# Optimization experiments

Measured on AMD Instinct MI355X. Metric: run time of the kernel, lower is better.

Reference implementation:

```python
import jax, jax.numpy as jnp
import numpy as np


def setup_inputs() -> dict:
    key = jax.random.key(0)
    k1, k2, k3 = jax.random.split(key, 3)
    B, N, L, H, E = 4, 4, 1024, 8, 64
    queries = jax.random.normal(k1, (B, N, L, H, E), dtype=jnp.float32)
    keys = jax.random.normal(k2, (B, N, L, H, E), dtype=jnp.float32)
    values = jax.random.normal(k3, (B, N, L, H, E), dtype=jnp.float32)
    return {"queries": queries, "keys": keys, "values": values}


def reference(queries, keys, values):
    B, N, L, H, E = queries.shape
    S = values.shape[2]
    scale = 1.0 / jnp.sqrt(jnp.asarray(E, queries.dtype))
    # scores: [B, N, H, L, S]
    scores = jnp.einsum('bnlhe,bnshe->bnhls', queries, keys)
    # causal mask: True above the diagonal (future positions), broadcast over b,n,h
    causal = jnp.triu(jnp.ones((L, S), dtype=bool), k=1)
    scores = jnp.where(causal, -jnp.inf, scores)
    A = jax.nn.softmax(scale * scores, axis=-1)  # dropout p=0.0 -> identity
    V = jnp.einsum('bnhls,bnshd->bnlhd', A, values)
    return V
```

## Files before the change

kernel.cpp:

```cpp
#include <hip/hip_runtime.h>
#include <hip/hip_bf16.h>


typedef __bf16 bf16x8 __attribute__((ext_vector_type(8)));
typedef __bf16 bf16x4 __attribute__((ext_vector_type(4)));
typedef float  f32x4  __attribute__((ext_vector_type(4)));
typedef unsigned u32x2 __attribute__((ext_vector_type(2)));
typedef unsigned u32x4 __attribute__((ext_vector_type(4)));

#define SEQ 1024
#define ROWSTRIDE 512

__device__ inline bf16x8 pack8(float4 a, float4 b) {
    bf16x8 f;
    f[0]=(__bf16)a.x; f[1]=(__bf16)a.y; f[2]=(__bf16)a.z; f[3]=(__bf16)a.w;
    f[4]=(__bf16)b.x; f[5]=(__bf16)b.y; f[6]=(__bf16)b.z; f[7]=(__bf16)b.w;
    return f;
}

__device__ inline bf16x8 pack8s(float4 a, float4 b, float s) {
    bf16x8 f;
    f[0]=(__bf16)(a.x*s); f[1]=(__bf16)(a.y*s); f[2]=(__bf16)(a.z*s); f[3]=(__bf16)(a.w*s);
    f[4]=(__bf16)(b.x*s); f[5]=(__bf16)(b.y*s); f[6]=(__bf16)(b.z*s); f[7]=(__bf16)(b.w*s);
    return f;
}

__device__ inline void lds_barrier() {
    asm volatile("s_waitcnt lgkmcnt(0)\n\ts_barrier" ::: "memory");
}

__device__ inline void swap32(unsigned &a, unsigned &b) {
    asm("v_permlane32_swap_b32 %0, %1" : "+v"(a), "+v"(b));
}
__device__ inline void swap16(unsigned &a, unsigned &b) {
    asm("v_permlane16_swap_b32 %0, %1" : "+v"(a), "+v"(b));
}

__global__ __launch_bounds__(256) void attn_fwd(
    const float* __restrict__ Qg,
    const float* __restrict__ Kg,
    const float* __restrict__ Vg,
    float* __restrict__ Og)
{
    __shared__ __bf16 Kds[2][64][64];
    __shared__ __bf16 Vds[2][64][64];

    const int blk  = blockIdx.x;
    const int pr   = blk >> 7;
    const int head = blk & 127;
    const int h    = head & 7;
    const int bn   = head >> 3;
    const int qts[2] = { pr, 15 - pr };

    const int tid  = threadIdx.x;
    const int wave = tid >> 6;
    const int lane = tid & 63;
    const int quad = lane >> 4;
    const int l15  = lane & 15;
    const int swz  = l15 & 7;

    const size_t base = (size_t)bn * SEQ * ROWSTRIDE + (size_t)h * 64;

    const float kscale = 0.125f * 1.44269504088896f;

    bf16x8 qa[2][2];
    int qrow[2];
    #pragma unroll
    for (int st = 0; st < 2; ++st) {
        qrow[st] = qts[st] * 64 + wave * 16;
        const float* qp = Qg + base + (size_t)(qrow[st] + l15) * ROWSTRIDE + quad * 8;
        #pragma unroll
        for (int t = 0; t < 2; ++t)
            qa[st][t] = pack8s(*(const float4*)(qp + t * 32),
                               *(const float4*)(qp + t * 32 + 4), kscale);
    }

    f32x4 o[2][4];
    float lsum[2];
    #pragma unroll
    for (int st = 0; st < 2; ++st) {
        #pragma unroll
        for (int e = 0; e < 4; ++e) o[st][e] = (f32x4){0.f, 0.f, 0.f, 0.f};
        lsum[st] = 0.f;
    }

    const int sr = tid >> 2, cbk = (tid & 3) << 1;
    const int ve = tid & 63, cbv = (tid >> 6) << 1;

    const int ntiles = qts[1] + 1;

    const float* kbase = Kg + base;
    const float* vbase = Vg + base;

    float4 kpre[4];
    float  vpre[16];
    {
        const float* kp = kbase + (size_t)sr * ROWSTRIDE + (cbk << 3);
        #pragma unroll
        for (int i = 0; i < 4; ++i) kpre[i] = *(const float4*)(kp + i * 4);
        const float* vp = vbase + (size_t)(cbv << 3) * ROWSTRIDE + ve;
        #pragma unroll
        for (int j = 0; j < 16; ++j) vpre[j] = vp[(size_t)j * ROWSTRIDE];
    }

    for (int tile = 0; tile < ntiles; ++tile) {
        const int bb = tile & 1;

        {
            const int rk = sr & 7;
            *(bf16x8*)&Kds[bb][sr][(cbk ^ rk) << 3]       = pack8(kpre[0], kpre[1]);
            *(bf16x8*)&Kds[bb][sr][((cbk + 1) ^ rk) << 3] = pack8(kpre[2], kpre[3]);
            bf16x8 f0, f1;
            #pragma unroll
            for (int jj = 0; jj < 8; ++jj) { f0[jj] = (__bf16)vpre[jj]; f1[jj] = (__bf16)vpre[8 + jj]; }
            const int rv = ve & 7;
            *(bf16x8*)&Vds[bb][ve][(cbv ^ rv) << 3]       = f0;
            *(bf16x8*)&Vds[bb][ve][((cbv + 1) ^ rv) << 3] = f1;
        }

        if (tile + 1 < ntiles) {
            const int s0n = (tile + 1) << 6;
            const float* kp = kbase + (size_t)(s0n + sr) * ROWSTRIDE + (cbk << 3);
            #pragma unroll
            for (int i = 0; i < 4; ++i) kpre[i] = *(const float4*)(kp + i * 4);
            const float* vp = vbase + (size_t)(s0n + (cbv << 3)) * ROWSTRIDE + ve;
            #pragma unroll
            for (int j = 0; j < 16; ++j) vpre[j] = vp[(size_t)j * ROWSTRIDE];
        }

        lds_barrier();

        bf16x8 pf[2][2];
        #pragma unroll
        for (int st = 0; st < 2; ++st) {
            if (tile > qts[st]) continue;
            f32x4 sacc[4];
            __builtin_amdgcn_s_setprio(1);
            #pragma unroll
            for (int c = 0; c < 4; ++c) {
                sacc[c] = (f32x4){0.f, 0.f, 0.f, 0.f};
                #pragma unroll
                for (int t = 0; t < 2; ++t) {
                    bf16x8 kb = *(const bf16x8*)&Kds[bb][c * 16 + l15][((t * 4 + quad) ^ swz) << 3];
                    sacc[c] = __builtin_amdgcn_mfma_f32_16x16x32_bf16(kb, qa[st][t], sacc[c], 0, 0, 0);
                }
            }
            __builtin_amdgcn_s_setprio(0);
            const bool diag = (tile == qts[st]);
            const int qin = wave * 16 + l15;
            float ls = 0.f;
            unsigned U[4][2];
            #pragma unroll
            for (int c = 0; c < 4; ++c) {
                bf16x4 pk;
                #pragma unroll
                for (int r = 0; r < 4; ++r) {
                    float p = __builtin_amdgcn_exp2f(sacc[c][r]);
                    if (diag && (c * 16 + quad * 4 + r > qin)) p = 0.f;
                    ls += p;
                    pk[r] = (__bf16)p;
                }
                u32x2 uu = __builtin_bit_cast(u32x2, pk);
                U[c][0] = uu[0]; U[c][1] = uu[1];
            }
            lsum[st] += ls;
            #pragma unroll
            for (int t = 0; t < 2; ++t) {
                unsigned a0 = U[2 * t][0], a1 = U[2 * t][1];
                unsigned b0 = U[2 * t + 1][0], b1 = U[2 * t + 1][1];
                swap32(a0, b0); swap32(a1, b1);
                swap16(a0, b0); swap16(a1, b1);
                u32x4 w; w[0] = a0; w[1] = a1; w[2] = b0; w[3] = b1;
                pf[st][t] = __builtin_bit_cast(bf16x8, w);
            }
        }

        const bool both = (tile <= qts[0]);
        __builtin_amdgcn_s_setprio(1);
        #pragma unroll
        for (int e = 0; e < 4; ++e) {
            #pragma unroll
            for (int t = 0; t < 2; ++t) {
                bf16x8 vb = *(const bf16x8*)&Vds[bb][e * 16 + l15][((t * 4 + quad) ^ swz) << 3];
                if (both)
                    o[0][e] = __builtin_amdgcn_mfma_f32_16x16x32_bf16(vb, pf[0][t], o[0][e], 0, 0, 0);
                o[1][e] = __builtin_amdgcn_mfma_f32_16x16x32_bf16(vb, pf[1][t], o[1][e], 0, 0, 0);
            }
        }
        __builtin_amdgcn_s_setprio(0);
    }

    #pragma unroll
    for (int st = 0; st < 2; ++st) {
        float s = lsum[st];
        s += __shfl_xor(s, 16);
        s += __shfl_xor(s, 32);
        const float inv_l = 1.f / s;
        float* op = Og + base + (size_t)(qrow[st] + l15) * ROWSTRIDE + quad * 4;
        #pragma unroll
        for (int e = 0; e < 4; ++e) {
            float4 v;
            v.x = o[st][e][0] * inv_l;
            v.y = o[st][e][1] * inv_l;
            v.z = o[st][e][2] * inv_l;
            v.w = o[st][e][3] * inv_l;
            *(float4*)(op + e * 16) = v;
        }
    }
}

extern "C" void kernel_launch(void* const* d_in, const int* in_sizes, int n_in,
                              void* d_out, int out_size, void* d_ws, size_t ws_size,
                              hipStream_t stream) {
    const float* Qg = (const float*)d_in[0];
    const float* Kg = (const float*)d_in[1];
    const float* Vg = (const float*)d_in[2];
    float* Og = (float*)d_out;
    attn_fwd<<<dim3(1024), dim3(256), 0, stream>>>(Qg, Kg, Vg, Og);
}
```

Before: 162.6 us.

## Split paired query tiles into separate blocks with 32-row KV tiles

Replaces the paired-query-tile scheme, where each block handled tiles pr and 15-pr, with one 64-row query tile per block and 2048 blocks. The KV tile shrinks to 32 rows and the V LDS layout and swizzle change to match. Per-wave causal skipping now leaves out fully masked 32-key subtiles. Launch bounds request 8 blocks per CU for higher occupancy. In exchange it loses load balancing between blocks and re-reads K/V once per query tile instead of once per pair.

After: 207.4 us. 1.28x slower.

```diff
diff --git a/kernel.cpp b/kernel.cpp
--- a/kernel.cpp
+++ b/kernel.cpp
@@ -10,6 +10,7 @@
 
 #define SEQ 1024
 #define ROWSTRIDE 512
+#define KVB 32
 
 __device__ inline bf16x8 pack8(float4 a, float4 b) {
     bf16x8 f;
@@ -36,21 +37,20 @@
     asm("v_permlane16_swap_b32 %0, %1" : "+v"(a), "+v"(b));
 }
 
-__global__ __launch_bounds__(256) void attn_fwd(
+__global__ __launch_bounds__(256, 8) void attn_fwd(
     const float* __restrict__ Qg,
     const float* __restrict__ Kg,
     const float* __restrict__ Vg,
     float* __restrict__ Og)
 {
-    __shared__ __bf16 Kds[2][64][64];
-    __shared__ __bf16 Vds[2][64][64];
+    __shared__ __bf16 Kds[2][KVB][64];
+    __shared__ __bf16 Vds[2][64][KVB];
 
     const int blk  = blockIdx.x;
-    const int pr   = blk >> 7;
+    const int qt   = blk >> 7;
     const int head = blk & 127;
     const int h    = head & 7;
     const int bn   = head >> 3;
-    const int qts[2] = { pr, 15 - pr };
 
     const int tid  = threadIdx.x;
     const int wave = tid >> 6;
@@ -58,152 +58,134 @@
     const int quad = lane >> 4;
     const int l15  = lane & 15;
     const int swz  = l15 & 7;
+    const int vswz = (l15 >> 1) & 3;
 
     const size_t base = (size_t)bn * SEQ * ROWSTRIDE + (size_t)h * 64;
 
     const float kscale = 0.125f * 1.44269504088896f;
 
-    bf16x8 qa[2][2];
-    int qrow[2];
-    #pragma unroll
-    for (int st = 0; st < 2; ++st) {
-        qrow[st] = qts[st] * 64 + wave * 16;
-        const float* qp = Qg + base + (size_t)(qrow[st] + l15) * ROWSTRIDE + quad * 8;
+    const int qrow = qt * 64 + wave * 16;
+    bf16x8 qa[2];
+    {
+        const float* qp = Qg + base + (size_t)(qrow + l15) * ROWSTRIDE + quad * 8;
         #pragma unroll
         for (int t = 0; t < 2; ++t)
-            qa[st][t] = pack8s(*(const float4*)(qp + t * 32),
-                               *(const float4*)(qp + t * 32 + 4), kscale);
+            qa[t] = pack8s(*(const float4*)(qp + t * 32),
+                           *(const float4*)(qp + t * 32 + 4), kscale);
     }
 
-    f32x4 o[2][4];
-    float lsum[2];
+    f32x4 o[4];
+    float lsum = 0.f;
     #pragma unroll
-    for (int st = 0; st < 2; ++st) {
-        #pragma unroll
-        for (int e = 0; e < 4; ++e) o[st][e] = (f32x4){0.f, 0.f, 0.f, 0.f};
-        lsum[st] = 0.f;
-    }
-
-    const int sr = tid >> 2, cbk = (tid & 3) << 1;
-    const int ve = tid & 63, cbv = (tid >> 6) << 1;
-
-    const int ntiles = qts[1] + 1;
-
-    const float* kbase = Kg + base;
-    const float* vbase = Vg + base;
-
-    float4 kpre[4];
-    float  vpre[16];
-    {
-        const float* kp = kbase + (size_t)sr * ROWSTRIDE + (cbk << 3);
-        #pragma unroll
-        for (int i = 0; i < 4; ++i) kpre[i] = *(const float4*)(kp + i * 4);
-        const float* vp = vbase + (size_t)(cbv << 3) * ROWSTRIDE + ve;
-        #pragma unroll
-        for (int j = 0; j < 16; ++j) vpre[j] = vp[(size_t)j * ROWSTRIDE];
-    }
+    for (int e = 0; e < 4; ++e) o[e] = (f32x4){0.f, 0.f, 0.f, 0.f};
+
+    const int sr = tid >> 3, kc = tid & 7;
+    const int ve = tid & 63;
+
+    const int ntiles = 2 * qt + 2;
+
+    const float* kp = Kg + base + (size_t)sr * ROWSTRIDE + kc * 8;
+    const float* vp = Vg + base + (size_t)(wave * 8) * ROWSTRIDE + ve;
+
+    float4 kpre[2];
+    float  vpre[8];
+    kpre[0] = *(const float4*)kp;
+    kpre[1] = *(const float4*)(kp + 4);
+    #pragma unroll
+    for (int j = 0; j < 8; ++j) vpre[j] = vp[(size_t)j * ROWSTRIDE];
+    kp += (size_t)KVB * ROWSTRIDE;
+    vp += (size_t)KVB * ROWSTRIDE;
 
     for (int tile = 0; tile < ntiles; ++tile) {
         const int bb = tile & 1;
 
+        *(bf16x8*)&Kds[bb][sr][(kc ^ (sr & 7)) << 3] = pack8(kpre[0], kpre[1]);
         {
-            const int rk = sr & 7;
-            *(bf16x8*)&Kds[bb][sr][(cbk ^ rk) << 3]       = pack8(kpre[0], kpre[1]);
-            *(bf16x8*)&Kds[bb][sr][((cbk + 1) ^ rk) << 3] = pack8(kpre[2], kpre[3]);
-            bf16x8 f0, f1;
-            #pragma unroll
-            for (int jj = 0; jj < 8; ++jj) { f0[jj] = (__bf16)vpre[jj]; f1[jj] = (__bf16)vpre[8 + jj]; }
-            const int rv = ve & 7;
-            *(bf16x8*)&Vds[bb][ve][(cbv ^ rv) << 3]       = f0;
-            *(bf16x8*)&Vds[bb][ve][((cbv + 1) ^ rv) << 3] = f1;
-        }
-
-        if (tile + 1 < ntiles) {
-            const int s0n = (tile + 1) << 6;
-            const float* kp = kbase + (size_t)(s0n + sr) * ROWSTRIDE + (cbk << 3);
-            #pragma unroll
-            for (int i = 0; i < 4; ++i) kpre[i] = *(const float4*)(kp + i * 4);
-            const float* vp = vbase + (size_t)(s0n + (cbv << 3)) * ROWSTRIDE + ve;
-            #pragma unroll
-            for (int j = 0; j < 16; ++j) vpre[j] = vp[(size_t)j * ROWSTRIDE];
+            bf16x8 f0;
+            #pragma unroll
+            for (int jj = 0; jj < 8; ++jj) f0[jj] = (__bf16)vpre[jj];
+            *(bf16x8*)&Vds[bb][ve][(wave ^ ((ve >> 1) & 3)) << 3] = f0;
         }
 
         lds_barrier();
 
-        bf16x8 pf[2][2];
-        #pragma unroll
-        for (int st = 0; st < 2; ++st) {
-            if (tile > qts[st]) continue;
-            f32x4 sacc[4];
+        const int reltile = tile * 32 - qt * 64 - wave * 16;
+        const bool active = reltile < 16;
+
+        bf16x8 pf;
+        if (active) {
+            f32x4 sacc[2];
             __builtin_amdgcn_s_setprio(1);
             #pragma unroll
-            for (int c = 0; c < 4; ++c) {
+            for (int c = 0; c < 2; ++c) {
                 sacc[c] = (f32x4){0.f, 0.f, 0.f, 0.f};
                 #pragma unroll
                 for (int t = 0; t < 2; ++t) {
                     bf16x8 kb = *(const bf16x8*)&Kds[bb][c * 16 + l15][((t * 4 + quad) ^ swz) << 3];
-                    sacc[c] = __builtin_amdgcn_mfma_f32_16x16x32_bf16(kb, qa[st][t], sacc[c], 0, 0, 0);
+                    sacc[c] = __builtin_amdgcn_mfma_f32_16x16x32_bf16(kb, qa[t], sacc[c], 0, 0, 0);
                 }
             }
             __builtin_amdgcn_s_setprio(0);
-            const bool diag = (tile == qts[st]);
-            const int qin = wave * 16 + l15;
+
+            const bool diag = (reltile >= -16);
             float ls = 0.f;
-            unsigned U[4][2];
-            #pragma unroll
-            for (int c = 0; c < 4; ++c) {
+            unsigned U[2][2];
+            #pragma unroll
+            for (int c = 0; c < 2; ++c) {
                 bf16x4 pk;
                 #pragma unroll
                 for (int r = 0; r < 4; ++r) {
                     float p = __builtin_amdgcn_exp2f(sacc[c][r]);
-                    if (diag && (c * 16 + quad * 4 + r > qin)) p = 0.f;
+                    if (diag && (reltile + c * 16 + quad * 4 + r > l15)) p = 0.f;
                     ls += p;
                     pk[r] = (__bf16)p;
                 }
                 u32x2 uu = __builtin_bit_cast(u32x2, pk);
                 U[c][0] = uu[0]; U[c][1] = uu[1];
             }
-            lsum[st] += ls;
-            #pragma unroll
-            for (int t = 0; t < 2; ++t) {
-                unsigned a0 = U[2 * t][0], a1 = U[2 * t][1];
-                unsigned b0 = U[2 * t + 1][0], b1 = U[2 * t + 1][1];
-                swap32(a0, b0); swap32(a1, b1);
-                swap16(a0, b0); swap16(a1, b1);
-                u32x4 w; w[0] = a0; w[1] = a1; w[2] = b0; w[3] = b1;
-                pf[st][t] = __builtin_bit_cast(bf16x8, w);
+            lsum += ls;
+
+            unsigned a0 = U[0][0], a1 = U[0][1];
+            unsigned b0 = U[1][0], b1 = U[1][1];
+            swap32(a0, b0); swap32(a1, b1);
+            swap16(a0, b0); swap16(a1, b1);
+            u32x4 w; w[0] = a0; w[1] = a1; w[2] = b0; w[3] = b1;
+            pf = __builtin_bit_cast(bf16x8, w);
+        }
+
+        if (tile + 1 < ntiles) {
+            kpre[0] = *(const float4*)kp;
+            kpre[1] = *(const float4*)(kp + 4);
+            #pragma unroll
+            for (int j = 0; j < 8; ++j) vpre[j] = vp[(size_t)j * ROWSTRIDE];
+            kp += (size_t)KVB * ROWSTRIDE;
+            vp += (size_t)KVB * ROWSTRIDE;
+        }
+
+        if (active) {
+            __builtin_amdgcn_s_setprio(1);
+            #pragma unroll
+            for (int e = 0; e < 4; ++e) {
+                bf16x8 vb = *(const bf16x8*)&Vds[bb][e * 16 + l15][(quad ^ vswz) << 3];
+                o[e] = __builtin_amdgcn_mfma_f32_16x16x32_bf16(vb, pf, o[e], 0, 0, 0);
             }
-        }
-
-        const bool both = (tile <= qts[0]);
-        __builtin_amdgcn_s_setprio(1);
-        #pragma unroll
-        for (int e = 0; e < 4; ++e) {
-            #pragma unroll
-            for (int t = 0; t < 2; ++t) {
-                bf16x8 vb = *(const bf16x8*)&Vds[bb][e * 16 + l15][((t * 4 + quad) ^ swz) << 3];
-                if (both)
-                    o[0][e] = __builtin_amdgcn_mfma_f32_16x16x32_bf16(vb, pf[0][t], o[0][e], 0, 0, 0);
-                o[1][e] = __builtin_amdgcn_mfma_f32_16x16x32_bf16(vb, pf[1][t], o[1][e], 0, 0, 0);
-            }
-        }
-        __builtin_amdgcn_s_setprio(0);
+            __builtin_amdgcn_s_setprio(0);
+        }
     }
 
-    #pragma unroll
-    for (int st = 0; st < 2; ++st) {
-        float s = lsum[st];
+    {
+        float s = lsum;
         s += __shfl_xor(s, 16);
         s += __shfl_xor(s, 32);
         const float inv_l = 1.f / s;
-        float* op = Og + base + (size_t)(qrow[st] + l15) * ROWSTRIDE + quad * 4;
+        float* op = Og + base + (size_t)(qrow + l15) * ROWSTRIDE + quad * 4;
         #pragma unroll
         for (int e = 0; e < 4; ++e) {
             float4 v;
-            v.x = o[st][e][0] * inv_l;
-            v.y = o[st][e][1] * inv_l;
-            v.z = o[st][e][2] * inv_l;
-            v.w = o[st][e][3] * inv_l;
+            v.x = o[e][0] * inv_l;
+            v.y = o[e][1] * inv_l;
+            v.z = o[e][2] * inv_l;
+            v.w = o[e][3] * inv_l;
             *(float4*)(op + e * 16) = v;
         }
     }
@@ -216,5 +198,5 @@
     const float* Kg = (const float*)d_in[1];
     const float* Vg = (const float*)d_in[2];
     float* Og = (float*)d_out;
-    attn_fwd<<<dim3(1024), dim3(256), 0, stream>>>(Qg, Kg, Vg, Og);
-}
+    attn_fwd<<<dim3(2048), dim3(256), 0, stream>>>(Qg, Kg, Vg, Og);
+}
```

## Replace paired-tile balancing with 128-row query tiles and per-wave causal skipping

Applied to the files above, without the earlier changes.

Each block now handles one contiguous 128-row query tile (32 rows per wave) instead of a balanced pair of 64-row tiles, and loops over 2*qt+2 key tiles. Each wave processes key tiles in 32-column phases and skips phases and PV MFMAs that lie entirely above its diagonal, so K fragments are reused across two query sub-tiles. This drops the front/back pairing that balanced work across blocks. Blocks now carry very different amounts of work, which may leave a long tail of late-running blocks.

Measured after the change: 155.5 us. 4.4% less time.

```diff
diff --git a/kernel.cpp b/kernel.cpp
--- a/kernel.cpp
+++ b/kernel.cpp
@@ -46,11 +46,10 @@
     __shared__ __bf16 Vds[2][64][64];
 
     const int blk  = blockIdx.x;
-    const int pr   = blk >> 7;
+    const int qt   = blk >> 7;
     const int head = blk & 127;
     const int h    = head & 7;
     const int bn   = head >> 3;
-    const int qts[2] = { pr, 15 - pr };
 
     const int tid  = threadIdx.x;
     const int wave = tid >> 6;
@@ -63,45 +62,40 @@
 
     const float kscale = 0.125f * 1.44269504088896f;
 
+    const int qrow = qt * 128 + wave * 32;
     bf16x8 qa[2][2];
-    int qrow[2];
-    #pragma unroll
-    for (int st = 0; st < 2; ++st) {
-        qrow[st] = qts[st] * 64 + wave * 16;
-        const float* qp = Qg + base + (size_t)(qrow[st] + l15) * ROWSTRIDE + quad * 8;
+    #pragma unroll
+    for (int qh = 0; qh < 2; ++qh) {
+        const float* qp = Qg + base + (size_t)(qrow + qh * 16 + l15) * ROWSTRIDE + quad * 8;
         #pragma unroll
         for (int t = 0; t < 2; ++t)
-            qa[st][t] = pack8s(*(const float4*)(qp + t * 32),
+            qa[qh][t] = pack8s(*(const float4*)(qp + t * 32),
                                *(const float4*)(qp + t * 32 + 4), kscale);
     }
 
     f32x4 o[2][4];
-    float lsum[2];
-    #pragma unroll
-    for (int st = 0; st < 2; ++st) {
+    float lsum[2] = {0.f, 0.f};
+    #pragma unroll
+    for (int qh = 0; qh < 2; ++qh)
         #pragma unroll
-        for (int e = 0; e < 4; ++e) o[st][e] = (f32x4){0.f, 0.f, 0.f, 0.f};
-        lsum[st] = 0.f;
-    }
+        for (int e = 0; e < 4; ++e) o[qh][e] = (f32x4){0.f, 0.f, 0.f, 0.f};
 
     const int sr = tid >> 2, cbk = (tid & 3) << 1;
     const int ve = tid & 63, cbv = (tid >> 6) << 1;
 
-    const int ntiles = qts[1] + 1;
-
-    const float* kbase = Kg + base;
-    const float* vbase = Vg + base;
+    const int ntiles = 2 * qt + 2;
+
+    const float* kp = Kg + base + (size_t)sr * ROWSTRIDE + (cbk << 3);
+    const float* vp = Vg + base + (size_t)(cbv << 3) * ROWSTRIDE + ve;
 
     float4 kpre[4];
     float  vpre[16];
-    {
-        const float* kp = kbase + (size_t)sr * ROWSTRIDE + (cbk << 3);
-        #pragma unroll
-        for (int i = 0; i < 4; ++i) kpre[i] = *(const float4*)(kp + i * 4);
-        const float* vp = vbase + (size_t)(cbv << 3) * ROWSTRIDE + ve;
-        #pragma unroll
-        for (int j = 0; j < 16; ++j) vpre[j] = vp[(size_t)j * ROWSTRIDE];
-    }
+    #pragma unroll
+    for (int i = 0; i < 4; ++i) kpre[i] = *(const float4*)(kp + i * 4);
+    #pragma unroll
+    for (int j = 0; j < 16; ++j) vpre[j] = vp[(size_t)j * ROWSTRIDE];
+    kp += (size_t)64 * ROWSTRIDE;
+    vp += (size_t)64 * ROWSTRIDE;
 
     for (int tile = 0; tile < ntiles; ++tile) {
         const int bb = tile & 1;
@@ -119,91 +113,114 @@
         }
 
         if (tile + 1 < ntiles) {
-            const int s0n = (tile + 1) << 6;
-            const float* kp = kbase + (size_t)(s0n + sr) * ROWSTRIDE + (cbk << 3);
             #pragma unroll
             for (int i = 0; i < 4; ++i) kpre[i] = *(const float4*)(kp + i * 4);
-            const float* vp = vbase + (size_t)(s0n + (cbv << 3)) * ROWSTRIDE + ve;
             #pragma unroll
             for (int j = 0; j < 16; ++j) vpre[j] = vp[(size_t)j * ROWSTRIDE];
+            kp += (size_t)64 * ROWSTRIDE;
+            vp += (size_t)64 * ROWSTRIDE;
         }
 
         lds_barrier();
 
+        const int relq = tile * 64 - qrow;
+        const bool active   = relq < 32;
+        const bool hiActive = relq < 0;
+
         bf16x8 pf[2][2];
-        #pragma unroll
-        for (int st = 0; st < 2; ++st) {
-            if (tile > qts[st]) continue;
-            f32x4 sacc[4];
+
+        auto phase = [&](int ph) {
+            f32x4 sacc[2][2];
+            #pragma unroll
+            for (int qh = 0; qh < 2; ++qh)
+                #pragma unroll
+                for (int cl = 0; cl < 2; ++cl) sacc[qh][cl] = (f32x4){0.f, 0.f, 0.f, 0.f};
             __builtin_amdgcn_s_setprio(1);
             #pragma unroll
-            for (int c = 0; c < 4; ++c) {
-                sacc[c] = (f32x4){0.f, 0.f, 0.f, 0.f};
+            for (int cl = 0; cl < 2; ++cl) {
                 #pragma unroll
                 for (int t = 0; t < 2; ++t) {
-                    bf16x8 kb = *(const bf16x8*)&Kds[bb][c * 16 + l15][((t * 4 + quad) ^ swz) << 3];
-                    sacc[c] = __builtin_amdgcn_mfma_f32_16x16x32_bf16(kb, qa[st][t], sacc[c], 0, 0, 0);
+                    bf16x8 kb = *(const bf16x8*)&Kds[bb][(ph * 2 + cl) * 16 + l15][((t * 4 + quad) ^ swz) << 3];
+                    sacc[0][cl] = __builtin_amdgcn_mfma_f32_16x16x32_bf16(kb, qa[0][t], sacc[0][cl], 0, 0, 0);
+                    sacc[1][cl] = __builtin_amdgcn_mfma_f32_16x16x32_bf16(kb, qa[1][t], sacc[1][cl], 0, 0, 0);
                 }
             }
             __builtin_amdgcn_s_setprio(0);
-            const bool diag = (tile == qts[st]);
-            const int qin = wave * 16 + l15;
-            float ls = 0.f;
-            unsigned U[4][2];
-            #pragma unroll
-            for (int c = 0; c < 4; ++c) {
-                bf16x4 pk;
-                #pragma unroll
-                for (int r = 0; r < 4; ++r) {
-                    float p = __builtin_amdgcn_exp2f(sacc[c][r]);
-                    if (diag && (c * 16 + quad * 4 + r > qin)) p = 0.f;
-                    ls += p;
-                    pk[r] = (__bf16)p;
+            const int pm = relq + ph * 32;
+            #pragma unroll
+            for (int qh = 0; qh < 2; ++qh) {
+                unsigned U[2][2];
+                float ls = 0.f;
+                if (pm == 0) {
+                    #pragma unroll
+                    for (int cl = 0; cl < 2; ++cl) {
+                        bf16x4 pk;
+                        #pragma unroll
+                        for (int r = 0; r < 4; ++r) {
+                            float p = __builtin_amdgcn_exp2f(sacc[qh][cl][r]);
+                            if (cl * 16 + quad * 4 + r > qh * 16 + l15) p = 0.f;
+                            ls += p; pk[r] = (__bf16)p;
+                        }
+                        u32x2 uu = __builtin_bit_cast(u32x2, pk);
+                        U[cl][0] = uu[0]; U[cl][1] = uu[1];
+                    }
+                } else {
+                    #pragma unroll
+                    for (int cl = 0; cl < 2; ++cl) {
+                        bf16x4 pk;
+                        #pragma unroll
+                        for (int r = 0; r < 4; ++r) {
+                            float p = __builtin_amdgcn_exp2f(sacc[qh][cl][r]);
+                            ls += p; pk[r] = (__bf16)p;
+                        }
+                        u32x2 uu = __builtin_bit_cast(u32x2, pk);
+                        U[cl][0] = uu[0]; U[cl][1] = uu[1];
+                    }
                 }
-                u32x2 uu = __builtin_bit_cast(u32x2, pk);
-                U[c][0] = uu[0]; U[c][1] = uu[1];
-            }
-            lsum[st] += ls;
-            #pragma unroll
-            for (int t = 0; t < 2; ++t) {
-                unsigned a0 = U[2 * t][0], a1 = U[2 * t][1];
-                unsigned b0 = U[2 * t + 1][0], b1 = U[2 * t + 1][1];
+                lsum[qh] += ls;
+                unsigned a0 = U[0][0], a1 = U[0][1];
+                unsigned b0 = U[1][0], b1 = U[1][1];
                 swap32(a0, b0); swap32(a1, b1);
                 swap16(a0, b0); swap16(a1, b1);
                 u32x4 w; w[0] = a0; w[1] = a1; w[2] = b0; w[3] = b1;
-                pf[st][t] = __builtin_bit_cast(bf16x8, w);
+                pf[qh][ph] = __builtin_bit_cast(bf16x8, w);
             }
-        }
-
-        const bool both = (tile <= qts[0]);
-        __builtin_amdgcn_s_setprio(1);
-        #pragma unroll
-        for (int e = 0; e < 4; ++e) {
-            #pragma unroll
-            for (int t = 0; t < 2; ++t) {
-                bf16x8 vb = *(const bf16x8*)&Vds[bb][e * 16 + l15][((t * 4 + quad) ^ swz) << 3];
-                if (both)
-                    o[0][e] = __builtin_amdgcn_mfma_f32_16x16x32_bf16(vb, pf[0][t], o[0][e], 0, 0, 0);
-                o[1][e] = __builtin_amdgcn_mfma_f32_16x16x32_bf16(vb, pf[1][t], o[1][e], 0, 0, 0);
+        };
+
+        if (active) {
+            phase(0);
+            if (hiActive) phase(1);
+
+            __builtin_amdgcn_s_setprio(1);
+            #pragma unroll
+            for (int e = 0; e < 4; ++e) {
+                bf16x8 vb0 = *(const bf16x8*)&Vds[bb][e * 16 + l15][(quad ^ swz) << 3];
+                o[0][e] = __builtin_amdgcn_mfma_f32_16x16x32_bf16(vb0, pf[0][0], o[0][e], 0, 0, 0);
+                o[1][e] = __builtin_amdgcn_mfma_f32_16x16x32_bf16(vb0, pf[1][0], o[1][e], 0, 0, 0);
+                if (hiActive) {
+                    bf16x8 vb1 = *(const bf16x8*)&Vds[bb][e * 16 + l15][((4 + quad) ^ swz) << 3];
+                    o[0][e] = __builtin_amdgcn_mfma_f32_16x16x32_bf16(vb1, pf[0][1], o[0][e], 0, 0, 0);
+                    o[1][e] = __builtin_amdgcn_mfma_f32_16x16x32_bf16(vb1, pf[1][1], o[1][e], 0, 0, 0);
+                }
             }
-        }
-        __builtin_amdgcn_s_setprio(0);
+            __builtin_amdgcn_s_setprio(0);
+        }
     }
 
     #pragma unroll
-    for (int st = 0; st < 2; ++st) {
-        float s = lsum[st];
+    for (int qh = 0; qh < 2; ++qh) {
+        float s = lsum[qh];
         s += __shfl_xor(s, 16);
         s += __shfl_xor(s, 32);
         const float inv_l = 1.f / s;
-        float* op = Og + base + (size_t)(qrow[st] + l15) * ROWSTRIDE + quad * 4;
+        float* op = Og + base + (size_t)(qrow + qh * 16 + l15) * ROWSTRIDE + quad * 4;
         #pragma unroll
         for (int e = 0; e < 4; ++e) {
             float4 v;
-            v.x = o[st][e][0] * inv_l;
-            v.y = o[st][e][1] * inv_l;
-            v.z = o[st][e][2] * inv_l;
-            v.w = o[st][e][3] * inv_l;
+            v.x = o[qh][e][0] * inv_l;
+            v.y = o[qh][e][1] * inv_l;
+            v.z = o[qh][e][2] * inv_l;
+            v.w = o[qh][e][3] * inv_l;
             *(float4*)(op + e * 16) = v;
         }
     }
```
